# Kernel tuning notes

Hardware: AMD Instinct MI355X
Metric: run time of the kernel (lower is better)

## Reference

```python
import jax, jax.numpy as jnp
import numpy as np

B_, L_, H_, P_ = 8, 4096, 512, 256
DT_MIN, DT_MAX = 1e-3, 1e-1


def setup_inputs() -> dict:
    key = jax.random.key(0)
    ks = jax.random.split(key, 6)
    input_sequence = jax.random.normal(ks[0], (B_, L_, H_), jnp.float32)
    # Stable diagonal SSM eigenvalues (HiPPO-like): negative real, spread imaginary
    Lambda_re = -0.5 * jnp.ones((P_,), jnp.float32)
    Lambda_im = jnp.pi * jnp.arange(P_, dtype=jnp.float32)
    # B, C stored as real arrays with trailing real/imag channel, as in the module
    B = jax.random.normal(ks[1], (P_, H_, 2), jnp.float32) / np.sqrt(2.0 * H_)
    C = jax.random.normal(ks[2], (H_, P_, 2), jnp.float32) / np.sqrt(float(P_))
    D = jax.random.normal(ks[3], (H_,), jnp.float32)
    log_step = jax.random.uniform(ks[4], (P_,), jnp.float32,
                                  float(np.log(DT_MIN)), float(np.log(DT_MAX)))
    return dict(input_sequence=input_sequence, Lambda_re=Lambda_re,
                Lambda_im=Lambda_im, B=B, C=C, D=D, log_step=log_step)


def _scan_ssm(Lambda_bar, Bu):
    """Diagonal linear recurrence x_k = Lambda_bar * x_{k-1} + Bu_k via parallel scan.
    Lambda_bar: (P,) complex64; Bu: (L, P) complex64 -> xs: (L, P) complex64."""
    A = jnp.broadcast_to(Lambda_bar, Bu.shape)

    def binop(e_i, e_j):
        a_i, b_i = e_i
        a_j, b_j = e_j
        return a_j * a_i, a_j * b_i + b_j

    _, xs = jax.lax.associative_scan(binop, (A, Bu))
    return xs


def reference(input_sequence, Lambda_re, Lambda_im, B, C, D, log_step):
    # complex parameters (conj_sym=True, clip_eigs=False, zoh discretization)
    Lambda = (Lambda_re + 1j * Lambda_im).astype(jnp.complex64)        # (P,)
    B_tilde = (B[..., 0] + 1j * B[..., 1]).astype(jnp.complex64)       # (P, H)
    C_tilde = (C[..., 0] + 1j * C[..., 1]).astype(jnp.complex64)       # (H, P)
    step = jnp.exp(log_step)                                           # (P,)
    # ZOH: Lambda_bar = exp(Lambda*dt); B_bar = Lambda^{-1}(Lambda_bar - I) B
    Lambda_bar = jnp.exp(Lambda * step)                                # (P,)
    B_bar = ((1.0 / Lambda) * (Lambda_bar - 1.0))[:, None] * B_tilde   # (P, H)
    # project inputs into state space: (B, L, P)
    Bu = jnp.einsum('blh,ph->blp', input_sequence.astype(jnp.complex64), B_bar)
    xs = jax.vmap(lambda bu: _scan_ssm(Lambda_bar, bu))(Bu)            # (B, L, P)
    state = xs[:, -1, :]                                               # (B, P)
    # conj_sym=True -> output uses 2 * Re(C x)
    ys = 2.0 * jnp.einsum('blp,hp->blh', xs, C_tilde).real             # (B, L, H)
    out = ys + D * input_sequence                                      # D-skip
    return out, state
```

## Files before the change

kernel.cpp:

```cpp
#include <hip/hip_runtime.h>
#include <hip/hip_bf16.h>

#define Hh 512
#define Pp 256
#define Ll 4096
#define Bb 8
#define BL (Bb*Ll)
#define Sc 64
#define NC 64

typedef __attribute__((ext_vector_type(8))) __bf16 bf16x8;
typedef __attribute__((ext_vector_type(4))) float  floatx4;

#define LAM_OFF     0
#define LAMS64D_OFF 512
#define B1G_OFF     1024
#define B3G_OFF     (B1G_OFF + 65536)
#define UB16_OFF    (B3G_OFF + 65536)
#define BUB_OFF     (UB16_OFF + 4194304)
#define XSB_OFF     (BUB_OFF + 4194304)
#define AGG_OFF     (XSB_OFF + 4194304)

#define LAMS16D_OFF XSB_OFF
#define AGG16_OFF   (XSB_OFF + 512)

#define OUT_ELEMS 16777216

#define GLL16(g, l) __builtin_amdgcn_global_load_lds( \
    (const __attribute__((address_space(1))) void*)(g), \
    (__attribute__((address_space(3))) void*)(l), 16, 0, 0)

#define BAR_LGKM()  asm volatile("s_waitcnt lgkmcnt(0)\n\ts_barrier" ::: "memory")
#define BAR_VMN(n)  asm volatile("s_waitcnt vmcnt(" #n ")\n\ts_barrier" ::: "memory")

__device__ __forceinline__ float2 cmul(float2 a, float2 b) {
    return make_float2(a.x*b.x - a.y*b.y, a.x*b.y + a.y*b.x);
}
__device__ __forceinline__ void cfma(float2& acc, float2 a, float2 b) {
    acc.x = fmaf(a.x, b.x, acc.x); acc.x = fmaf(-a.y, b.y, acc.x);
    acc.y = fmaf(a.x, b.y, acc.y); acc.y = fmaf( a.y, b.x, acc.y);
}

__global__ void prep(const float* __restrict__ u,
                     const float* __restrict__ Bmat, const float* __restrict__ Cmat,
                     const float* __restrict__ Lre, const float* __restrict__ Lim,
                     const float* __restrict__ logstep, float2* __restrict__ ws) {
    int bid = blockIdx.x;
    if (bid < 8192) {
        long i = ((long)bid * 256 + threadIdx.x) * 8;
        float4 v0 = *(const float4*)(u + i);
        float4 v1 = *(const float4*)(u + i + 4);
        __align__(16) __hip_bfloat162 t[4];
        t[0] = __float22bfloat162_rn(make_float2(v0.x, v0.y));
        t[1] = __float22bfloat162_rn(make_float2(v0.z, v0.w));
        t[2] = __float22bfloat162_rn(make_float2(v1.x, v1.y));
        t[3] = __float22bfloat162_rn(make_float2(v1.z, v1.w));
        *(bf16x8*)((__hip_bfloat16*)(ws + UB16_OFF) + i) = *(const bf16x8*)t;
    } else if (bid < 8704) {
        int idx = (bid - 8192) * 256 + threadIdx.x;
        int p = idx >> 9, h = idx & 511;
        double lr = (double)Lre[p], li = (double)Lim[p];
        double st = exp((double)logstep[p]);
        double a  = lr * st, th = li * st;
        double er = exp(a);
        double lamr = er * cos(th), lami = er * sin(th);
        double nr = lamr - 1.0, ni = lami;
        double den = lr*lr + li*li;
        float gx = (float)((nr*lr + ni*li)/den), gy = (float)((ni*lr - nr*li)/den);
        float2 b = ((const float2*)Bmat)[idx];
        float re = gx*b.x - gy*b.y;
        float im = gx*b.y + gy*b.x;
        __hip_bfloat16* B1 = (__hip_bfloat16*)(ws + B1G_OFF);
        B1[(2*p)*512 + h]   = __float2bfloat16(re);
        B1[(2*p+1)*512 + h] = __float2bfloat16(im);
    } else if (bid < 9216) {
        int idx = (bid - 8704) * 256 + threadIdx.x;
        int h = idx >> 8, p = idx & 255;
        float2 c = ((const float2*)Cmat)[idx];
        __hip_bfloat162* B3 = (__hip_bfloat162*)(ws + B3G_OFF);
        B3[h*256 + p] = __float22bfloat162_rn(make_float2(2.f*c.x, -2.f*c.y));
    } else {
        int p = threadIdx.x;
        double lr = (double)Lre[p], li = (double)Lim[p];
        double st = exp((double)logstep[p]);
        double a  = lr * st, th = li * st;
        double er = exp(a);
        ws[LAM_OFF + p] = make_float2((float)(er*cos(th)), (float)(er*sin(th)));
        double er64 = exp(64.0 * a), th64 = 64.0 * th;
        ((double2*)(ws + LAMS64D_OFF))[p] = make_double2(er64*cos(th64), er64*sin(th64));
        double er16 = exp(16.0 * a), th16 = 16.0 * th;
        ((double2*)(ws + LAMS16D_OFF))[p] = make_double2(er16*cos(th16), er16*sin(th16));
    }
}

#define STAGE(buf, kt) do { \
    _Pragma("unroll") \
    for (int h_ = 0; h_ < 2; ++h_) { \
        _Pragma("unroll") \
        for (int r_ = 0; r_ < 2; ++r_) { \
            GLL16(aSrc + (h_*128 + r_*64)*1024 + (kt)*128, \
                  ldsSt + (buf)*65536 + h_*16384 + r_*8192); \
            GLL16(bSrc + (h_*128 + r_*64)*1024 + (kt)*128, \
                  ldsSt + (buf)*65536 + 32768 + h_*16384 + r_*8192); \
        } \
    } \
} while (0)

__global__ __launch_bounds__(512, 2)
void gemm1(const __hip_bfloat16* __restrict__ A,
           const __hip_bfloat16* __restrict__ B,
           void* __restrict__ Cout,
           const float2* __restrict__ lamTab,
           float2* __restrict__ aggOut,
           float2* __restrict__ agg16Out) {
    __shared__ __align__(16) char lds[131072];
    const int tid = threadIdx.x;
    const int w = tid >> 6, l = tid & 63;

    const int idx = blockIdx.x;
    const int swz = (idx & 7) * 32 + (idx >> 3);
    const int mt = swz >> 1, nt = swz & 1;
    const long M0 = (long)mt * 256;
    const int  N0 = nt * 256;

    const int rA  = l >> 3;
    const int csw = ((l & 7) ^ rA) * 16;
    const char* aSrc = (const char*)A + (M0 + w*8 + rA) * 1024 + csw;
    const char* bSrc = (const char*)B + (long)(N0 + w*8 + rA) * 1024 + csw;
    char* ldsSt = lds + w*1024 + l*16;

    const int quad = l >> 4, ml = l & 15, m7 = ml & 7;
    const int wm = w & 1, wn = w >> 1;
    const int o0 = ((quad    ) ^ m7) * 16;
    const int o1 = ((quad + 4) ^ m7) * 16;
    const char* aRd = lds + wm*16384 + ml*128;
    const char* bRd = lds + 32768 + wn*8192 + ml*128;

    floatx4 acc[8][4];
    #pragma unroll
    for (int i = 0; i < 8; ++i)
        #pragma unroll
        for (int j = 0; j < 4; ++j) acc[i][j] = (floatx4)0.f;

    STAGE(0, 0);
    STAGE(1, 1);
    BAR_VMN(8);

    #pragma unroll
    for (int t = 0; t < 8; ++t) {
        const int tb = (t & 1) * 65536;
        {
            bf16x8 af[8], bfr[4];
            #pragma unroll
            for (int fm = 0; fm < 8; ++fm)
                af[fm] = *(const bf16x8*)(aRd + tb + fm*2048 + o0);
            #pragma unroll
            for (int fn = 0; fn < 4; ++fn)
                bfr[fn] = *(const bf16x8*)(bRd + tb + fn*2048 + o0);
            __builtin_amdgcn_s_setprio(1);
            #pragma unroll
            for (int fm = 0; fm < 8; ++fm)
                #pragma unroll
                for (int fn = 0; fn < 4; ++fn)
                    acc[fm][fn] = __builtin_amdgcn_mfma_f32_16x16x32_bf16(
                        af[fm], bfr[fn], acc[fm][fn], 0, 0, 0);
            __builtin_amdgcn_s_setprio(0);
        }
        {
            bf16x8 af[8], bfr[4];
            #pragma unroll
            for (int fm = 0; fm < 8; ++fm)
                af[fm] = *(const bf16x8*)(aRd + tb + fm*2048 + o1);
            #pragma unroll
            for (int fn = 0; fn < 4; ++fn)
                bfr[fn] = *(const bf16x8*)(bRd + tb + fn*2048 + o1);
            BAR_LGKM();
            if (t + 2 < 8) STAGE(t & 1, t + 2);
            __builtin_amdgcn_sched_barrier(0);
            __builtin_amdgcn_s_setprio(1);
            #pragma unroll
            for (int fm = 0; fm < 8; ++fm)
                #pragma unroll
                for (int fn = 0; fn < 4; ++fn)
                    acc[fm][fn] = __builtin_amdgcn_mfma_f32_16x16x32_bf16(
                        af[fm], bfr[fn], acc[fm][fn], 0, 0, 0);
            __builtin_amdgcn_s_setprio(0);
        }
        if (t < 6)       BAR_VMN(8);
        else if (t == 6) BAR_VMN(0);
    }

    const int b   = (int)(M0 >> 12);
    const int gc0 = (int)((M0 >> 6) & 63);
    #pragma unroll
    for (int fn = 0; fn < 4; ++fn) {
        const int col = N0 + wn*64 + fn*16 + ml;
        const int p = col >> 1;
        const float2 lam = lamTab[p];
        const float2 one = make_float2(1.f, 0.f);
        const float2 l2  = cmul(lam, lam);
        const float2 l3  = cmul(l2, lam);
        const float2 l4  = cmul(l2, l2);
        const float2 l8  = cmul(l4, l4);
        const float2 l12 = cmul(l8, l4);
        const float2 l16 = cmul(l8, l8);
        const float2 l32 = cmul(l16, l16);
        const float2 l48 = cmul(l32, l16);
        const float2 P4q = (quad==3) ? one : (quad==2) ? l4 : (quad==1) ? l8 : l12;
        #pragma unroll
        for (int c = 0; c < 2; ++c) {
            float2 sc = make_float2(0.f, 0.f);
            #pragma unroll
            for (int a = 0; a < 4; ++a) {
                const int fm = c*4 + a;
                float vr[4];
                #pragma unroll
                for (int reg = 0; reg < 4; ++reg) {
                    const long row = M0 + wm*128 + fm*16 + quad*4 + reg;
                    __hip_bfloat16 hv = __float2bfloat16(acc[fm][fn][reg]);
                    ((__hip_bfloat16*)Cout)[row * 512 + col] = hv;
                    vr[reg] = __bfloat162float(hv);
                }
                float2 s;
                s.x = fmaf(l3.x, vr[0], fmaf(l2.x, vr[1], fmaf(lam.x, vr[2], vr[3])));
                s.y = fmaf(l3.y, vr[0], fmaf(l2.y, vr[1], lam.y * vr[2]));
                const float2 p16 = (a==3) ? one : (a==2) ? l16 : (a==1) ? l32 : l48;
                cfma(sc, cmul(p16, P4q), s);
                float2 tq = cmul(P4q, s);
                tq.x += __shfl_xor(tq.x, 16); tq.y += __shfl_xor(tq.y, 16);
                tq.x += __shfl_xor(tq.x, 32); tq.y += __shfl_xor(tq.y, 32);
                const float tox = __shfl_xor(tq.x, 1);
                const float toy = __shfl_xor(tq.y, 1);
                if (quad == 0 && (ml & 1) == 0)
                    agg16Out[((size_t)((b*NC + gc0 + wm*2 + c)*4 + a))*Pp + p] =
                        make_float2(tq.x - toy, tq.y + tox);
            }
            sc.x += __shfl_xor(sc.x, 16); sc.y += __shfl_xor(sc.y, 16);
            sc.x += __shfl_xor(sc.x, 32); sc.y += __shfl_xor(sc.y, 32);
            const float ox = __shfl_xor(sc.x, 1);
            const float oy = __shfl_xor(sc.y, 1);
            if (quad == 0 && (ml & 1) == 0) {
                aggOut[(b*NC + gc0 + wm*2 + c) * Pp + p] =
                    make_float2(sc.x - oy, sc.y + ox);
            }
        }
    }
}

#define STAGEA2(buf, kt) do { \
    _Pragma("unroll") \
    for (int h_ = 0; h_ < 2; ++h_) { \
        _Pragma("unroll") \
        for (int r_ = 0; r_ < 2; ++r_) { \
            GLL16(aSrc + (h_*128 + r_*64)*1024 + (kt)*128, \
                  ldsA + (buf)*32768 + h_*16384 + r_*8192); \
        } \
    } \
} while (0)
#define STAGEB2(buf, kt) do { \
    _Pragma("unroll") \
    for (int h_ = 0; h_ < 2; ++h_) { \
        _Pragma("unroll") \
        for (int r_ = 0; r_ < 2; ++r_) { \
            GLL16(bSrc + (h_*128 + r_*64)*1024 + (kt)*128, \
                  ldsB + (buf)*32768 + h_*16384 + r_*8192); \
        } \
    } \
} while (0)

#define SCAN_TILE(ktC, bufA) do { \
    const int s16_ = tid >> 5; \
    const float2 lam_ = lamK[ktC]; \
    float2 x_ = carry16L[s16_*256 + (ktC)*32 + p5g]; \
    char* base_ = lds + (bufA)*32768; \
    _Pragma("unroll") \
    for (int jj_ = 0; jj_ < 16; ++jj_) { \
        const int j_ = (s16_ << 4) + jj_; \
        char* cell_ = base_ + j_*128 + ((((p5g >> 2) ^ (j_ & 7)) << 4) | ((p5g & 3) << 2)); \
        float2 v_ = __bfloat1622float2(*(const __hip_bfloat162*)cell_); \
        float nr_ = fmaf(lam_.x, x_.x, v_.x); nr_ = fmaf(-lam_.y, x_.y, nr_); \
        float ni_ = fmaf(lam_.x, x_.y, v_.y); ni_ = fmaf( lam_.y, x_.x, ni_); \
        x_.x = nr_; x_.y = ni_; \
        *(__hip_bfloat162*)cell_ = __float22bfloat162_rn(x_); \
    } \
    if (s16_ == 15 && gc0 == 60 && nt == 0) { \
        out[OUT_ELEMS + b * Pp + (ktC)*32 + p5g] = x_.x; \
        out[OUT_ELEMS + Bb * Pp + b * Pp + (ktC)*32 + p5g] = x_.y; \
    } \
} while (0)

__global__ __launch_bounds__(512, 2)
void gemm2f(const __hip_bfloat16* __restrict__ A,
            const __hip_bfloat16* __restrict__ Bg,
            float* __restrict__ out,
            const __hip_bfloat16* __restrict__ ub,
            const float* __restrict__ Dv,
            const float2* __restrict__ lamTab,
            const double2* __restrict__ lam64,
            const double2* __restrict__ lam16,
            const float2* __restrict__ agg,
            const float2* __restrict__ agg16) {
    __shared__ __align__(16) char lds[163840];
    const int tid = threadIdx.x;
    const int w = tid >> 6, l = tid & 63;
    const int idx = blockIdx.x;
    const int swz = (idx & 7) * 32 + (idx >> 3);
    const int mt = swz >> 1, nt = swz & 1;
    const long M0 = (long)mt * 256;
    const int  N0 = nt * 256;
    const int b   = (int)(M0 >> 12);
    const int gc0 = (int)((M0 >> 6) & 63);

    const int rA  = l >> 3;
    const int csw = ((l & 7) ^ rA) * 16;
    const char* aSrc = (const char*)A + (M0 + w*8 + rA) * 1024 + csw;
    const char* bSrc = (const char*)Bg + (long)(N0 + w*8 + rA) * 1024 + csw;
    char* ldsA = lds + w*1024 + l*16;
    char* ldsB = lds + 65536 + w*1024 + l*16;

    const int quad = l >> 4, ml = l & 15, m7 = ml & 7;
    const int wm = w & 1, wn = w >> 1;
    const int o0 = ((quad    ) ^ m7) * 16;
    const int o1 = ((quad + 4) ^ m7) * 16;
    const char* aRd = lds + wm*16384 + ml*128;
    const char* bRd = lds + 65536 + wn*8192 + ml*128;
    float2* carry16L = (float2*)(lds + 131072);

    const int p5g = tid & 31;
    float2 lamK[8];
    #pragma unroll
    for (int kt = 0; kt < 8; ++kt) lamK[kt] = lamTab[kt*32 + p5g];

    STAGEA2(0, 0); STAGEB2(0, 0);
    STAGEA2(1, 1); STAGEB2(1, 1);

    if (tid < 256) {
        const int p = tid;
        const double2 l64 = lam64[p];
        const double2 l16 = lam16[p];
        double cr = 0.0, ci = 0.0;
        for (int cp = 0; cp + 4 <= gc0; cp += 4) {
            float2 a0 = agg[(b*NC + cp    ) * Pp + p];
            float2 a1 = agg[(b*NC + cp + 1) * Pp + p];
            float2 a2 = agg[(b*NC + cp + 2) * Pp + p];
            float2 a3 = agg[(b*NC + cp + 3) * Pp + p];
            double nr, ni;
            nr = fma(l64.x, cr, (double)a0.x); nr = fma(-l64.y, ci, nr);
            ni = fma(l64.x, ci, (double)a0.y); ni = fma( l64.y, cr, ni); cr = nr; ci = ni;
            nr = fma(l64.x, cr, (double)a1.x); nr = fma(-l64.y, ci, nr);
            ni = fma(l64.x, ci, (double)a1.y); ni = fma( l64.y, cr, ni); cr = nr; ci = ni;
            nr = fma(l64.x, cr, (double)a2.x); nr = fma(-l64.y, ci, nr);
            ni = fma(l64.x, ci, (double)a2.y); ni = fma( l64.y, cr, ni); cr = nr; ci = ni;
            nr = fma(l64.x, cr, (double)a3.x); nr = fma(-l64.y, ci, nr);
            ni = fma(l64.x, ci, (double)a3.y); ni = fma( l64.y, cr, ni); cr = nr; ci = ni;
        }
        #pragma unroll
        for (int ch = 0; ch < 4; ++ch) {
            carry16L[(ch*4 + 0)*256 + p] = make_float2((float)cr, (float)ci);
            double scr = cr, sci = ci;
            #pragma unroll
            for (int sq = 1; sq < 4; ++sq) {
                float2 a16 = agg16[((size_t)((b*NC + gc0 + ch)*4 + (sq-1)))*Pp + p];
                double nr = fma(l16.x, scr, (double)a16.x); nr = fma(-l16.y, sci, nr);
                double ni = fma(l16.x, sci, (double)a16.y); ni = fma( l16.y, scr, ni);
                scr = nr; sci = ni;
                carry16L[(ch*4 + sq)*256 + p] = make_float2((float)scr, (float)sci);
            }
            if (ch < 3) {
                float2 a = agg[(b*NC + gc0 + ch) * Pp + p];
                double nr = fma(l64.x, cr, (double)a.x); nr = fma(-l64.y, ci, nr);
                double ni = fma(l64.x, ci, (double)a.y); ni = fma( l64.y, cr, ni);
                cr = nr; ci = ni;
            }
        }
    }
    asm volatile("s_waitcnt vmcnt(8) lgkmcnt(0)\n\ts_barrier" ::: "memory");
    SCAN_TILE(0, 0);
    BAR_LGKM();

    floatx4 acc[8][4];
    #pragma unroll
    for (int i = 0; i < 8; ++i)
        #pragma unroll
        for (int j = 0; j < 4; ++j) acc[i][j] = (floatx4)0.f;

    #pragma unroll
    for (int kt = 0; kt < 8; ++kt) {
        const int cb = kt & 1;
        const int tb = cb * 32768;
        {
            bf16x8 af[8], bfr[4];
            #pragma unroll
            for (int fm = 0; fm < 8; ++fm)
                af[fm] = *(const bf16x8*)(aRd + tb + fm*2048 + o0);
            #pragma unroll
            for (int fn = 0; fn < 4; ++fn)
                bfr[fn] = *(const bf16x8*)(bRd + tb + fn*2048 + o0);
            __builtin_amdgcn_s_setprio(1);
            #pragma unroll
            for (int fm = 0; fm < 8; ++fm)
                #pragma unroll
                for (int fn = 0; fn < 4; ++fn)
                    acc[fm][fn] = __builtin_amdgcn_mfma_f32_16x16x32_bf16(
                        af[fm], bfr[fn], acc[fm][fn], 0, 0, 0);
            __builtin_amdgcn_s_setprio(0);
        }
        {
            bf16x8 af[8], bfr[4];
            #pragma unroll
            for (int fm = 0; fm < 8; ++fm)
                af[fm] = *(const bf16x8*)(aRd + tb + fm*2048 + o1);
            #pragma unroll
            for (int fn = 0; fn < 4; ++fn)
                bfr[fn] = *(const bf16x8*)(bRd + tb + fn*2048 + o1);
            BAR_LGKM();
            if (kt + 2 < 8) { STAGEA2(cb, kt + 2); STAGEB2(cb, kt + 2); }
            __builtin_amdgcn_sched_barrier(0);
            __builtin_amdgcn_s_setprio(1);
            #pragma unroll
            for (int fm = 0; fm < 8; ++fm)
                #pragma unroll
                for (int fn = 0; fn < 4; ++fn)
                    acc[fm][fn] = __builtin_amdgcn_mfma_f32_16x16x32_bf16(
                        af[fm], bfr[fn], acc[fm][fn], 0, 0, 0);
            __builtin_amdgcn_s_setprio(0);
        }
        if (kt < 6)       { BAR_VMN(8); SCAN_TILE(kt + 1, cb ^ 1); BAR_LGKM(); }
        else if (kt == 6) { BAR_VMN(0); SCAN_TILE(7, cb ^ 1); BAR_LGKM(); }
    }

    #pragma unroll
    for (int fm = 0; fm < 8; ++fm)
        #pragma unroll
        for (int fn = 0; fn < 4; ++fn) {
            const int col = N0 + wn*64 + fn*16 + ml;
            const float d = Dv[col];
            #pragma unroll
            for (int reg = 0; reg < 4; ++reg) {
                const long row = M0 + wm*128 + fm*16 + quad*4 + reg;
                const long o = row * 512 + col;
                out[o] = acc[fm][fn][reg] + d * __bfloat162float(ub[o]);
            }
        }
}

extern "C" void kernel_launch(void* const* d_in, const int* in_sizes, int n_in,
                              void* d_out, int out_size, void* d_ws, size_t ws_size,
                              hipStream_t stream) {
    const float* u       = (const float*)d_in[0];
    const float* Lre     = (const float*)d_in[1];
    const float* Lim     = (const float*)d_in[2];
    const float* Bmat    = (const float*)d_in[3];
    const float* Cmat    = (const float*)d_in[4];
    const float* Dv      = (const float*)d_in[5];
    const float* logstep = (const float*)d_in[6];
    float*  out = (float*)d_out;
    float2* ws  = (float2*)d_ws;

    prep<<<9217, 256, 0, stream>>>(u, Bmat, Cmat, Lre, Lim, logstep, ws);

    gemm1<<<256, 512, 0, stream>>>(
        (const __hip_bfloat16*)(ws + UB16_OFF),
        (const __hip_bfloat16*)(ws + B1G_OFF),
        (void*)(ws + BUB_OFF),
        (const float2*)(ws + LAM_OFF),
        (float2*)(ws + AGG_OFF),
        (float2*)(ws + AGG16_OFF));

    gemm2f<<<256, 512, 0, stream>>>(
        (const __hip_bfloat16*)(ws + BUB_OFF),
        (const __hip_bfloat16*)(ws + B3G_OFF),
        out,
        (const __hip_bfloat16*)(ws + UB16_OFF), Dv,
        (const float2*)(ws + LAM_OFF),
        (const double2*)(ws + LAMS64D_OFF),
        (const double2*)(ws + LAMS16D_OFF),
        (const float2*)(ws + AGG_OFF),
        (const float2*)(ws + AGG16_OFF));
}
```

Baseline: 188.4 us.

## Double workgroup size to 1024 threads with 4x4 warp tiling in both GEMMs

```diff
diff --git a/kernel.cpp b/kernel.cpp
--- a/kernel.cpp
+++ b/kernel.cpp
@@ -96,17 +96,14 @@
 #define STAGE(buf, kt) do { \
     _Pragma("unroll") \
     for (int h_ = 0; h_ < 2; ++h_) { \
-        _Pragma("unroll") \
-        for (int r_ = 0; r_ < 2; ++r_) { \
-            GLL16(aSrc + (h_*128 + r_*64)*1024 + (kt)*128, \
-                  ldsSt + (buf)*65536 + h_*16384 + r_*8192); \
-            GLL16(bSrc + (h_*128 + r_*64)*1024 + (kt)*128, \
-                  ldsSt + (buf)*65536 + 32768 + h_*16384 + r_*8192); \
-        } \
+        GLL16(aSrc + (h_*128)*1024 + (kt)*128, \
+              ldsSt + (buf)*65536 + h_*16384); \
+        GLL16(bSrc + (h_*128)*1024 + (kt)*128, \
+              ldsSt + (buf)*65536 + 32768 + h_*16384); \
     } \
 } while (0)
 
-__global__ __launch_bounds__(512, 2)
+__global__ __launch_bounds__(1024)
 void gemm1(const __hip_bfloat16* __restrict__ A,
            const __hip_bfloat16* __restrict__ B,
            void* __restrict__ Cout,
@@ -130,36 +127,36 @@
     char* ldsSt = lds + w*1024 + l*16;
 
     const int quad = l >> 4, ml = l & 15, m7 = ml & 7;
-    const int wm = w & 1, wn = w >> 1;
+    const int wm = w & 3, wn = w >> 2;
     const int o0 = ((quad    ) ^ m7) * 16;
     const int o1 = ((quad + 4) ^ m7) * 16;
-    const char* aRd = lds + wm*16384 + ml*128;
+    const char* aRd = lds + wm*8192 + ml*128;
     const char* bRd = lds + 32768 + wn*8192 + ml*128;
 
-    floatx4 acc[8][4];
-    #pragma unroll
-    for (int i = 0; i < 8; ++i)
+    floatx4 acc[4][4];
+    #pragma unroll
+    for (int i = 0; i < 4; ++i)
         #pragma unroll
         for (int j = 0; j < 4; ++j) acc[i][j] = (floatx4)0.f;
 
     STAGE(0, 0);
     STAGE(1, 1);
-    BAR_VMN(8);
+    BAR_VMN(4);
 
     #pragma unroll
     for (int t = 0; t < 8; ++t) {
         const int tb = (t & 1) * 65536;
         {
-            bf16x8 af[8], bfr[4];
-            #pragma unroll
-            for (int fm = 0; fm < 8; ++fm)
+            bf16x8 af[4], bfr[4];
+            #pragma unroll
+            for (int fm = 0; fm < 4; ++fm)
                 af[fm] = *(const bf16x8*)(aRd + tb + fm*2048 + o0);
             #pragma unroll
             for (int fn = 0; fn < 4; ++fn)
                 bfr[fn] = *(const bf16x8*)(bRd + tb + fn*2048 + o0);
             __builtin_amdgcn_s_setprio(1);
             #pragma unroll
-            for (int fm = 0; fm < 8; ++fm)
+            for (int fm = 0; fm < 4; ++fm)
                 #pragma unroll
                 for (int fn = 0; fn < 4; ++fn)
                     acc[fm][fn] = __builtin_amdgcn_mfma_f32_16x16x32_bf16(
@@ -167,9 +164,9 @@
             __builtin_amdgcn_s_setprio(0);
         }
         {
-            bf16x8 af[8], bfr[4];
-            #pragma unroll
-            for (int fm = 0; fm < 8; ++fm)
+            bf16x8 af[4], bfr[4];
+            #pragma unroll
+            for (int fm = 0; fm < 4; ++fm)
                 af[fm] = *(const bf16x8*)(aRd + tb + fm*2048 + o1);
             #pragma unroll
             for (int fn = 0; fn < 4; ++fn)
@@ -179,19 +176,20 @@
             __builtin_amdgcn_sched_barrier(0);
             __builtin_amdgcn_s_setprio(1);
             #pragma unroll
-            for (int fm = 0; fm < 8; ++fm)
+            for (int fm = 0; fm < 4; ++fm)
                 #pragma unroll
                 for (int fn = 0; fn < 4; ++fn)
                     acc[fm][fn] = __builtin_amdgcn_mfma_f32_16x16x32_bf16(
                         af[fm], bfr[fn], acc[fm][fn], 0, 0, 0);
             __builtin_amdgcn_s_setprio(0);
         }
-        if (t < 6)       BAR_VMN(8);
+        if (t < 6)       BAR_VMN(4);
         else if (t == 6) BAR_VMN(0);
     }
 
     const int b   = (int)(M0 >> 12);
     const int gc0 = (int)((M0 >> 6) & 63);
+    const int gch = gc0 + wm;
     #pragma unroll
     for (int fn = 0; fn < 4; ++fn) {
         const int col = N0 + wn*64 + fn*16 + ml;
@@ -207,42 +205,37 @@
         const float2 l32 = cmul(l16, l16);
         const float2 l48 = cmul(l32, l16);
         const float2 P4q = (quad==3) ? one : (quad==2) ? l4 : (quad==1) ? l8 : l12;
+        float2 sc = make_float2(0.f, 0.f);
         #pragma unroll
-        for (int c = 0; c < 2; ++c) {
-            float2 sc = make_float2(0.f, 0.f);
-            #pragma unroll
-            for (int a = 0; a < 4; ++a) {
-                const int fm = c*4 + a;
-                float vr[4];
-                #pragma unroll
-                for (int reg = 0; reg < 4; ++reg) {
-                    const long row = M0 + wm*128 + fm*16 + quad*4 + reg;
-                    __hip_bfloat16 hv = __float2bfloat16(acc[fm][fn][reg]);
-                    ((__hip_bfloat16*)Cout)[row * 512 + col] = hv;
-                    vr[reg] = __bfloat162float(hv);
-                }
-                float2 s;
-                s.x = fmaf(l3.x, vr[0], fmaf(l2.x, vr[1], fmaf(lam.x, vr[2], vr[3])));
-                s.y = fmaf(l3.y, vr[0], fmaf(l2.y, vr[1], lam.y * vr[2]));
-                const float2 p16 = (a==3) ? one : (a==2) ? l16 : (a==1) ? l32 : l48;
-                cfma(sc, cmul(p16, P4q), s);
-                float2 tq = cmul(P4q, s);
-                tq.x += __shfl_xor(tq.x, 16); tq.y += __shfl_xor(tq.y, 16);
-                tq.x += __shfl_xor(tq.x, 32); tq.y += __shfl_xor(tq.y, 32);
-                const float tox = __shfl_xor(tq.x, 1);
-                const float toy = __shfl_xor(tq.y, 1);
-                if (quad == 0 && (ml & 1) == 0)
-                    agg16Out[((size_t)((b*NC + gc0 + wm*2 + c)*4 + a))*Pp + p] =
-                        make_float2(tq.x - toy, tq.y + tox);
+        for (int fm = 0; fm < 4; ++fm) {
+            float vr[4];
+            #pragma unroll
+            for (int reg = 0; reg < 4; ++reg) {
+                const long row = M0 + wm*64 + fm*16 + quad*4 + reg;
+                __hip_bfloat16 hv = __float2bfloat16(acc[fm][fn][reg]);
+                ((__hip_bfloat16*)Cout)[row * 512 + col] = hv;
+                vr[reg] = __bfloat162float(hv);
             }
-            sc.x += __shfl_xor(sc.x, 16); sc.y += __shfl_xor(sc.y, 16);
-            sc.x += __shfl_xor(sc.x, 32); sc.y += __shfl_xor(sc.y, 32);
-            const float ox = __shfl_xor(sc.x, 1);
-            const float oy = __shfl_xor(sc.y, 1);
-            if (quad == 0 && (ml & 1) == 0) {
-                aggOut[(b*NC + gc0 + wm*2 + c) * Pp + p] =
-                    make_float2(sc.x - oy, sc.y + ox);
-            }
+            float2 s;
+            s.x = fmaf(l3.x, vr[0], fmaf(l2.x, vr[1], fmaf(lam.x, vr[2], vr[3])));
+            s.y = fmaf(l3.y, vr[0], fmaf(l2.y, vr[1], lam.y * vr[2]));
+            const float2 p16 = (fm==3) ? one : (fm==2) ? l16 : (fm==1) ? l32 : l48;
+            cfma(sc, cmul(p16, P4q), s);
+            float2 tq = cmul(P4q, s);
+            tq.x += __shfl_xor(tq.x, 16); tq.y += __shfl_xor(tq.y, 16);
+            tq.x += __shfl_xor(tq.x, 32); tq.y += __shfl_xor(tq.y, 32);
+            const float tox = __shfl_xor(tq.x, 1);
+            const float toy = __shfl_xor(tq.y, 1);
+            if (quad == 0 && (ml & 1) == 0)
+                agg16Out[((size_t)((b*NC + gch)*4 + fm))*Pp + p] =
+                    make_float2(tq.x - toy, tq.y + tox);
+        }
+        sc.x += __shfl_xor(sc.x, 16); sc.y += __shfl_xor(sc.y, 16);
+        sc.x += __shfl_xor(sc.x, 32); sc.y += __shfl_xor(sc.y, 32);
+        const float ox = __shfl_xor(sc.x, 1);
+        const float oy = __shfl_xor(sc.y, 1);
+        if (quad == 0 && (ml & 1) == 0) {
+            aggOut[(b*NC + gch) * Pp + p] = make_float2(sc.x - oy, sc.y + ox);
         }
     }
 }
@@ -250,46 +243,42 @@
 #define STAGEA2(buf, kt) do { \
     _Pragma("unroll") \
     for (int h_ = 0; h_ < 2; ++h_) { \
-        _Pragma("unroll") \
-        for (int r_ = 0; r_ < 2; ++r_) { \
-            GLL16(aSrc + (h_*128 + r_*64)*1024 + (kt)*128, \
-                  ldsA + (buf)*32768 + h_*16384 + r_*8192); \
-        } \
+        GLL16(aSrc + (h_*128)*1024 + (kt)*128, \
+              ldsA + (buf)*32768 + h_*16384); \
     } \
 } while (0)
 #define STAGEB2(buf, kt) do { \
     _Pragma("unroll") \
     for (int h_ = 0; h_ < 2; ++h_) { \
+        GLL16(bSrc + (h_*128)*1024 + (kt)*128, \
+              ldsB + (buf)*32768 + h_*16384); \
+    } \
+} while (0)
+
+#define SCAN_TILE(ktC, bufA) do { \
+    if (tid < 512) { \
+        const int s16_ = tid >> 5; \
+        const float2 lam_ = lamK[ktC]; \
+        float2 x_ = carry16L[s16_*256 + (ktC)*32 + p5g]; \
+        char* base_ = lds + (bufA)*32768; \
         _Pragma("unroll") \
-        for (int r_ = 0; r_ < 2; ++r_) { \
-            GLL16(bSrc + (h_*128 + r_*64)*1024 + (kt)*128, \
-                  ldsB + (buf)*32768 + h_*16384 + r_*8192); \
+        for (int jj_ = 0; jj_ < 16; ++jj_) { \
+            const int j_ = (s16_ << 4) + jj_; \
+            char* cell_ = base_ + j_*128 + ((((p5g >> 2) ^ (j_ & 7)) << 4) | ((p5g & 3) << 2)); \
+            float2 v_ = __bfloat1622float2(*(const __hip_bfloat162*)cell_); \
+            float nr_ = fmaf(lam_.x, x_.x, v_.x); nr_ = fmaf(-lam_.y, x_.y, nr_); \
+            float ni_ = fmaf(lam_.x, x_.y, v_.y); ni_ = fmaf( lam_.y, x_.x, ni_); \
+            x_.x = nr_; x_.y = ni_; \
+            *(__hip_bfloat162*)cell_ = __float22bfloat162_rn(x_); \
+        } \
+        if (s16_ == 15 && gc0 == 60 && nt == 0) { \
+            out[OUT_ELEMS + b * Pp + (ktC)*32 + p5g] = x_.x; \
+            out[OUT_ELEMS + Bb * Pp + b * Pp + (ktC)*32 + p5g] = x_.y; \
         } \
     } \
 } while (0)
 
-#define SCAN_TILE(ktC, bufA) do { \
-    const int s16_ = tid >> 5; \
-    const float2 lam_ = lamK[ktC]; \
-    float2 x_ = carry16L[s16_*256 + (ktC)*32 + p5g]; \
-    char* base_ = lds + (bufA)*32768; \
-    _Pragma("unroll") \
-    for (int jj_ = 0; jj_ < 16; ++jj_) { \
-        const int j_ = (s16_ << 4) + jj_; \
-        char* cell_ = base_ + j_*128 + ((((p5g >> 2) ^ (j_ & 7)) << 4) | ((p5g & 3) << 2)); \
-        float2 v_ = __bfloat1622float2(*(const __hip_bfloat162*)cell_); \
-        float nr_ = fmaf(lam_.x, x_.x, v_.x); nr_ = fmaf(-lam_.y, x_.y, nr_); \
-        float ni_ = fmaf(lam_.x, x_.y, v_.y); ni_ = fmaf( lam_.y, x_.x, ni_); \
-        x_.x = nr_; x_.y = ni_; \
-        *(__hip_bfloat162*)cell_ = __float22bfloat162_rn(x_); \
-    } \
-    if (s16_ == 15 && gc0 == 60 && nt == 0) { \
-        out[OUT_ELEMS + b * Pp + (ktC)*32 + p5g] = x_.x; \
-        out[OUT_ELEMS + Bb * Pp + b * Pp + (ktC)*32 + p5g] = x_.y; \
-    } \
-} while (0)
-
-__global__ __launch_bounds__(512, 2)
+__global__ __launch_bounds__(1024)
 void gemm2f(const __hip_bfloat16* __restrict__ A,
             const __hip_bfloat16* __restrict__ Bg,
             float* __restrict__ out,
@@ -319,10 +308,10 @@
     char* ldsB = lds + 65536 + w*1024 + l*16;
 
     const int quad = l >> 4, ml = l & 15, m7 = ml & 7;
-    const int wm = w & 1, wn = w >> 1;
+    const int wm = w & 3, wn = w >> 2;
     const int o0 = ((quad    ) ^ m7) * 16;
     const int o1 = ((quad + 4) ^ m7) * 16;
-    const char* aRd = lds + wm*16384 + ml*128;
+    const char* aRd = lds + wm*8192 + ml*128;
     const char* bRd = lds + 65536 + wn*8192 + ml*128;
     float2* carry16L = (float2*)(lds + 131072);
 
@@ -374,13 +363,13 @@
             }
         }
     }
-    asm volatile("s_waitcnt vmcnt(8) lgkmcnt(0)\n\ts_barrier" ::: "memory");
+    asm volatile("s_waitcnt vmcnt(4) lgkmcnt(0)\n\ts_barrier" ::: "memory");
     SCAN_TILE(0, 0);
     BAR_LGKM();
 
-    floatx4 acc[8][4];
-    #pragma unroll
-    for (int i = 0; i < 8; ++i)
+    floatx4 acc[4][4];
+    #pragma unroll
+    for (int i = 0; i < 4; ++i)
         #pragma unroll
         for (int j = 0; j < 4; ++j) acc[i][j] = (floatx4)0.f;
 
@@ -389,16 +378,16 @@
         const int cb = kt & 1;
         const int tb = cb * 32768;
         {
-            bf16x8 af[8], bfr[4];
-            #pragma unroll
-            for (int fm = 0; fm < 8; ++fm)
+            bf16x8 af[4], bfr[4];
+            #pragma unroll
+            for (int fm = 0; fm < 4; ++fm)
                 af[fm] = *(const bf16x8*)(aRd + tb + fm*2048 + o0);
             #pragma unroll
             for (int fn = 0; fn < 4; ++fn)
                 bfr[fn] = *(const bf16x8*)(bRd + tb + fn*2048 + o0);
             __builtin_amdgcn_s_setprio(1);
             #pragma unroll
-            for (int fm = 0; fm < 8; ++fm)
+            for (int fm = 0; fm < 4; ++fm)
                 #pragma unroll
                 for (int fn = 0; fn < 4; ++fn)
                     acc[fm][fn] = __builtin_amdgcn_mfma_f32_16x16x32_bf16(
@@ -406,9 +395,9 @@
             __builtin_amdgcn_s_setprio(0);
         }
         {
-            bf16x8 af[8], bfr[4];
-            #pragma unroll
-            for (int fm = 0; fm < 8; ++fm)
+            bf16x8 af[4], bfr[4];
+            #pragma unroll
+            for (int fm = 0; fm < 4; ++fm)
                 af[fm] = *(const bf16x8*)(aRd + tb + fm*2048 + o1);
             #pragma unroll
             for (int fn = 0; fn < 4; ++fn)
@@ -418,26 +407,26 @@
             __builtin_amdgcn_sched_barrier(0);
             __builtin_amdgcn_s_setprio(1);
             #pragma unroll
-            for (int fm = 0; fm < 8; ++fm)
+            for (int fm = 0; fm < 4; ++fm)
                 #pragma unroll
                 for (int fn = 0; fn < 4; ++fn)
                     acc[fm][fn] = __builtin_amdgcn_mfma_f32_16x16x32_bf16(
                         af[fm], bfr[fn], acc[fm][fn], 0, 0, 0);
             __builtin_amdgcn_s_setprio(0);
         }
-        if (kt < 6)       { BAR_VMN(8); SCAN_TILE(kt + 1, cb ^ 1); BAR_LGKM(); }
+        if (kt < 6)       { BAR_VMN(4); SCAN_TILE(kt + 1, cb ^ 1); BAR_LGKM(); }
         else if (kt == 6) { BAR_VMN(0); SCAN_TILE(7, cb ^ 1); BAR_LGKM(); }
     }
 
     #pragma unroll
-    for (int fm = 0; fm < 8; ++fm)
+    for (int fm = 0; fm < 4; ++fm)
         #pragma unroll
         for (int fn = 0; fn < 4; ++fn) {
             const int col = N0 + wn*64 + fn*16 + ml;
             const float d = Dv[col];
             #pragma unroll
             for (int reg = 0; reg < 4; ++reg) {
-                const long row = M0 + wm*128 + fm*16 + quad*4 + reg;
+                const long row = M0 + wm*64 + fm*16 + quad*4 + reg;
                 const long o = row * 512 + col;
                 out[o] = acc[fm][fn][reg] + d * __bfloat162float(ub[o]);
             }
@@ -459,7 +448,7 @@
 
     prep<<<9217, 256, 0, stream>>>(u, Bmat, Cmat, Lre, Lim, logstep, ws);
 
-    gemm1<<<256, 512, 0, stream>>>(
+    gemm1<<<256, 1024, 0, stream>>>(
         (const __hip_bfloat16*)(ws + UB16_OFF),
         (const __hip_bfloat16*)(ws + B1G_OFF),
         (void*)(ws + BUB_OFF),
@@ -467,7 +456,7 @@
         (float2*)(ws + AGG_OFF),
         (float2*)(ws + AGG16_OFF));
 
-    gemm2f<<<256, 512, 0, stream>>>(
+    gemm2f<<<256, 1024, 0, stream>>>(
         (const __hip_bfloat16*)(ws + BUB_OFF),
         (const __hip_bfloat16*)(ws + B3G_OFF),
         out,
```

After: 209.1 us. +11.0%, slower.
